# Kernel tuning notes

Measured on AMD Instinct MI355X. Metric: run time of the kernel, lower is better.

Reference implementation:

```python
import jax, jax.numpy as jnp
import numpy as np

V, E, U, B, T = 50000, 128, 256, 256, 1024


def _lstm_cell(x, h, c, W, R, b):
    # Keras LSTMCell gate order: i, f, g(candidate), o
    z = x @ W + h @ R + b  # [B, 4U]
    i, f, g, o = jnp.split(z, 4, axis=-1)
    i = jax.nn.sigmoid(i)
    f = jax.nn.sigmoid(f)
    g = jnp.tanh(g)
    o = jax.nn.sigmoid(o)
    c_new = f * c + i * g
    h_new = o * jnp.tanh(c_new)
    return h_new, c_new


def setup_inputs() -> dict:
    key = jax.random.key(0)
    ks = jax.random.split(key, 10)
    s = lambda k, shape, scale: jax.random.normal(k, shape, dtype=jnp.float32) * scale
    return {
        "tokens": jax.random.randint(ks[0], (B, T), 0, V),
        "emb": s(ks[1], (V, E), 0.05),
        "W0": s(ks[2], (E, 4 * U), 1.0 / np.sqrt(E)),
        "R0": s(ks[3], (U, 4 * U), 1.0 / np.sqrt(U)),
        "b0": jnp.zeros((4 * U,), jnp.float32),
        "W1": s(ks[4], (U, 4 * U), 1.0 / np.sqrt(U)),
        "R1": s(ks[5], (U, 4 * U), 1.0 / np.sqrt(U)),
        "b1": jnp.zeros((4 * U,), jnp.float32),
        "Wout": s(ks[6], (U, 1), 1.0 / np.sqrt(U)),
        "bout": jnp.zeros((1,), jnp.float32),
    }


def reference(tokens, emb, W0, R0, b0, W1, R1, b1, Wout, bout):
    x = emb[tokens]                      # [B, T, E]
    xs = jnp.transpose(x, (1, 0, 2))     # [T, B, E] scan over time
    h0 = jnp.zeros((B, U), x.dtype)
    c0 = jnp.zeros((B, U), x.dtype)
    h1 = jnp.zeros((B, U), x.dtype)
    c1 = jnp.zeros((B, U), x.dtype)

    def step(carry, x_t):
        h0, c0, h1, c1 = carry
        h0, c0 = _lstm_cell(x_t, h0, c0, W0, R0, b0)
        h1, c1 = _lstm_cell(h0, h1, c1, W1, R1, b1)
        return (h0, c0, h1, c1), None

    (h0, c0, h1, c1), _ = jax.lax.scan(step, (h0, c0, h1, c1), xs)
    logits = h1 @ Wout + bout            # [B, 1]
    return jax.nn.sigmoid(logits)
```

## Files before the change

kernel.cpp:

```cpp
#include <hip/hip_runtime.h>

typedef unsigned short u16;
typedef unsigned int u32;
typedef unsigned long long u64;
typedef __attribute__((ext_vector_type(8))) short bf16x8;
typedef __attribute__((ext_vector_type(4))) float f32x4;

#define T_STEPS 1024
#define E_SZ 128
#define U_SZ 256

#define NG 16
#define MB 16
#define NSL 8
#define RD 8
#define HS 264
#define EPAD 136
#define BSTRIDE 192

#define POLL_BAIL 60000

#define L0_W0T 0
#define L0_R0T 32768
#define L0_X   98304
#define L0_STG 102656
#define L0_G   110848
#define L0_B   119616
#define L1_W1T 0
#define L1_R1T 65536
#define L1_SG0 131072
#define L1_SG1 139264
#define L1_G   147456
#define L1_B   156224
#define SMEM_TOTAL 156800

__device__ u64 g_exH0[RD * NG * NSL * BSTRIDE];
__device__ u64 g_exH1[2 * NG * NSL * BSTRIDE];
__device__ int g_pr[NG * NSL * 16];
__device__ u32 g_run;
__device__ int g_isF32;

__device__ __forceinline__ float bf2f(u16 u) {
  union { u32 i; float f; } v; v.i = ((u32)u) << 16; return v.f;
}
__device__ __forceinline__ u16 f2bf(float f) {
  union { u32 i; float f; } v; v.f = f;
  u32 r = v.i + 0x7fffu + ((v.i >> 16) & 1u);
  return (u16)(r >> 16);
}
__device__ __forceinline__ float sig_(float x) { return 1.f / (1.f + __expf(-x)); }
__device__ __forceinline__ float tnh_(float x) { return 2.f / (1.f + __expf(-2.f * x)) - 1.f; }

extern "C" __global__ void dtype_probe(const void* W0v) {
  __shared__ int cntBig;
  if (threadIdx.x == 0) cntBig = 0;
  __syncthreads();
  const u16* u = (const u16*)W0v;
  int big = 0;
  for (int i = threadIdx.x; i < 4096; i += 256)
    if ((u[i] & 0x7F80u) >= 0x4100u) big++;
  atomicAdd(&cntBig, big);
  __syncthreads();
  for (int i = threadIdx.x; i < NG * NSL * 16; i += 256) g_pr[i] = 0;
  if (threadIdx.x == 0) {
    g_isF32 = (cntBig > 100) ? 1 : 0;
    g_run = g_run + 1;
  }
}

__device__ __forceinline__ u64 ldAtom(const u64* p) {
  return __hip_atomic_load(p, __ATOMIC_RELAXED, __HIP_MEMORY_SCOPE_AGENT);
}

__device__ __forceinline__ int wavePollMin(const int* fA, int tgt, int lane,
                                           int& dead) {
  if (dead) return tgt;
  const int* p = (lane < 8) ? fA + lane * 16 : nullptr;
  int ok = (p == nullptr);
  int v = 0x7fffffff;
  int it = 0;
  while (!__all(ok)) {
    if (!ok) {
      v = __hip_atomic_load(p, __ATOMIC_RELAXED, __HIP_MEMORY_SCOPE_AGENT);
      ok = v >= tgt;
    }
    if (++it > POLL_BAIL) { dead = 1; break; }
    if (it > 48) __builtin_amdgcn_s_sleep(1);
  }
  __atomic_signal_fence(__ATOMIC_ACQUIRE);
  int m = (lane < 8) ? v : 0x7fffffff;
#pragma unroll
  for (int off = 4; off; off >>= 1) {
    int o = __shfl_down(m, off);
    m = m < o ? m : o;
  }
  return __shfl(m, 0);
}

__device__ __forceinline__ void unpackToLds(const u64 q0, const u64 q1, const u64 q2,
                                            u16* __restrict__ stg, int slice,
                                            int ml, int quad) {
  u32 a0 = (u32)q0, a1 = (u32)(q0 >> 32);
  u32 b0 = (u32)q1, b1 = (u32)(q1 >> 32);
  u32 c0 = (u32)q2;
  uint4 F;
  F.x = a0;
  F.y = (a1 & 0xFFFFu) | (b0 << 16);
  F.z = (b0 >> 16) | (b1 << 16);
  F.w = c0;
  *(uint4*)(stg + (((slice << 6) + (quad << 4) + ml) << 3)) = F;
}

__device__ __forceinline__ void stageOne(const u64* __restrict__ base, u32 etag,
                                         u16* __restrict__ stg,
                                         int wv, int ml, int quad, int& dead) {
  const int j0 = wv << 1;
  const u64* p0 = base + (u64)j0 * BSTRIDE + ml * 12 + quad * 3;
  const u64* p1 = p0 + BSTRIDE;
  u64 qa0 = ldAtom(p0), qa1 = ldAtom(p0 + 1), qa2 = ldAtom(p0 + 2);
  u64 qb0 = ldAtom(p1), qb1 = ldAtom(p1 + 1), qb2 = ldAtom(p1 + 2);
  int it = 0;
  while (true) {
    u32 badA = (((u32)(qa0 >> 48)) ^ etag) | (((u32)(qa1 >> 48)) ^ etag) |
               (((u32)(qa2 >> 48)) ^ etag);
    u32 badB = (((u32)(qb0 >> 48)) ^ etag) | (((u32)(qb1 >> 48)) ^ etag) |
               (((u32)(qb2 >> 48)) ^ etag);
    if (!__any((badA | badB) != 0)) break;
    if (dead) break;
    if (++it > POLL_BAIL) { dead = 1; break; }
    if (badA) { qa0 = ldAtom(p0); qa1 = ldAtom(p0 + 1); qa2 = ldAtom(p0 + 2); }
    if (badB) { qb0 = ldAtom(p1); qb1 = ldAtom(p1 + 1); qb2 = ldAtom(p1 + 2); }
    if (it > 8) __builtin_amdgcn_s_sleep(1);
  }
  __atomic_signal_fence(__ATOMIC_ACQUIRE);
  unpackToLds(qa0, qa1, qa2, stg, j0, ml, quad);
  unpackToLds(qb0, qb1, qb2, stg, j0 + 1, ml, quad);
}

__device__ __forceinline__ void stageDual(const u64* __restrict__ b0, u32 e0,
                                          u16* __restrict__ s0,
                                          const u64* __restrict__ b1, u32 e1,
                                          u16* __restrict__ s1, int doH1,
                                          int wv, int ml, int quad, int& dead) {
  const int j0 = wv << 1;
  const int off = ml * 12 + quad * 3;
  const u64* p0a = b0 + (u64)j0 * BSTRIDE + off;
  const u64* p0b = p0a + BSTRIDE;
  const u64* p1a = b1 + (u64)j0 * BSTRIDE + off;
  const u64* p1b = p1a + BSTRIDE;
  u64 xa0 = ldAtom(p0a), xa1 = ldAtom(p0a + 1), xa2 = ldAtom(p0a + 2);
  u64 xb0 = ldAtom(p0b), xb1 = ldAtom(p0b + 1), xb2 = ldAtom(p0b + 2);
  u64 ya0 = 0, ya1 = 0, ya2 = 0, yb0 = 0, yb1 = 0, yb2 = 0;
  if (doH1) {
    ya0 = ldAtom(p1a); ya1 = ldAtom(p1a + 1); ya2 = ldAtom(p1a + 2);
    yb0 = ldAtom(p1b); yb1 = ldAtom(p1b + 1); yb2 = ldAtom(p1b + 2);
  }
  int it = 0;
  while (true) {
    u32 badA = (((u32)(xa0 >> 48)) ^ e0) | (((u32)(xa1 >> 48)) ^ e0) |
               (((u32)(xa2 >> 48)) ^ e0);
    u32 badB = (((u32)(xb0 >> 48)) ^ e0) | (((u32)(xb1 >> 48)) ^ e0) |
               (((u32)(xb2 >> 48)) ^ e0);
    u32 badC = 0, badD = 0;
    if (doH1) {
      badC = (((u32)(ya0 >> 48)) ^ e1) | (((u32)(ya1 >> 48)) ^ e1) |
             (((u32)(ya2 >> 48)) ^ e1);
      badD = (((u32)(yb0 >> 48)) ^ e1) | (((u32)(yb1 >> 48)) ^ e1) |
             (((u32)(yb2 >> 48)) ^ e1);
    }
    if (!__any((badA | badB | badC | badD) != 0)) break;
    if (dead) break;
    if (++it > POLL_BAIL) { dead = 1; break; }
    if (badA) { xa0 = ldAtom(p0a); xa1 = ldAtom(p0a + 1); xa2 = ldAtom(p0a + 2); }
    if (badB) { xb0 = ldAtom(p0b); xb1 = ldAtom(p0b + 1); xb2 = ldAtom(p0b + 2); }
    if (badC) { ya0 = ldAtom(p1a); ya1 = ldAtom(p1a + 1); ya2 = ldAtom(p1a + 2); }
    if (badD) { yb0 = ldAtom(p1b); yb1 = ldAtom(p1b + 1); yb2 = ldAtom(p1b + 2); }
    if (it > 8) __builtin_amdgcn_s_sleep(1);
  }
  __atomic_signal_fence(__ATOMIC_ACQUIRE);
  unpackToLds(xa0, xa1, xa2, s0, j0, ml, quad);
  unpackToLds(xb0, xb1, xb2, s0, j0 + 1, ml, quad);
  if (doH1) {
    unpackToLds(ya0, ya1, ya2, s1, j0, ml, quad);
    unpackToLds(yb0, yb1, yb2, s1, j0 + 1, ml, quad);
  }
}

extern "C" __global__ void __launch_bounds__(256, 1)
lstm_fused(const int* __restrict__ tokens, const void* __restrict__ emb,
           const void* __restrict__ W0, const void* __restrict__ R0, const void* __restrict__ b0,
           const void* __restrict__ W1, const void* __restrict__ R1, const void* __restrict__ b1,
           const void* __restrict__ Wout, const void* __restrict__ bout,
           void* __restrict__ outv) {
  extern __shared__ char smem[];

  const int tid = threadIdx.x;
  const int b = blockIdx.x;
  const int g = b & (NG - 1);
  const int w = b >> 4;
  const int role = w >> 3;
  const int sl = w & 7;
  const int isF32 = g_isF32;
  const u32 tagB = ((u32)g_run) << 10;

  auto ldf = [&](const void* p, int idx) -> float {
    return isF32 ? ((const float*)p)[idx] : bf2f(((const u16*)p)[idx]);
  };

  const int lane = tid & 63;
  const int wv = tid >> 6;
  const int ml = lane & 15;
  const int quad = lane >> 4;
  const int um = tid >> 4;
  const int un = tid & 15;
  const int lfr = (quad << 4) + ml;

  const int mB = tid >> 4;
  const int uS = tid & 15;
  const int qS = uS / 3;
  const int sS = uS - qS * 3;
  const int kb = (qS << 3) + 3 * sS;
  const int nFull = (sS != 2);

  int* flp = g_pr + (g << 3) * 16;
  int dead = 0;

  if (role == 0) {
    u16* w0t = (u16*)(smem + L0_W0T);
    u16* r0t = (u16*)(smem + L0_R0T);
    u16* ldsX = (u16*)(smem + L0_X);
    u16* stg = (u16*)(smem + L0_STG);
    float* ldsG = (float*)(smem + L0_G);
    float* ldsB = (float*)(smem + L0_B);

    for (int i = tid; i < 128 * 128; i += 256) {
      int k = i >> 7, n = i & 127;
      int col = ((n >> 5) << 8) + (sl << 5) + (n & 31);
      int wv_ = n >> 5, s_ = (n >> 4) & 1, ml_ = n & 15;
      int j_ = k >> 5, q_ = (k >> 3) & 3, e_ = k & 7;
      int dst = ((((wv_ << 1) + s_) * 4 + j_) * 64 + (q_ << 4) + ml_) * 8 + e_;
      w0t[dst] = f2bf(ldf(W0, k * 1024 + col));
    }
    for (int i = tid; i < 128 * 256; i += 256) {
      int k = i >> 7, n = i & 127;
      int col = ((n >> 5) << 8) + (sl << 5) + (n & 31);
      int wv_ = n >> 5, s_ = (n >> 4) & 1, ml_ = n & 15;
      int j_ = k >> 5, q_ = (k >> 3) & 3, e_ = k & 7;
      int dst = ((((wv_ << 1) + s_) * 8 + j_) * 64 + (q_ << 4) + ml_) * 8 + e_;
      r0t[dst] = f2bf(ldf(R0, k * 1024 + col));
    }
    if (tid < 128) {
      int col = ((tid >> 5) << 8) + (sl << 5) + (tid & 31);
      ldsB[tid] = ldf(b0, col);
    }

    float cst[3] = {0.f, 0.f, 0.f};
    const int tokBase = (g * MB + um) * T_STEPS;
    int prMin = 0;

    float4 xfA, xfB; uint4 xbf;
    {
      int tok = tokens[tokBase];
      if (isF32) {
        const float* row = (const float*)emb + (u64)tok * E_SZ + (un << 3);
        xfA = *(const float4*)row; xfB = *(const float4*)(row + 4);
      } else {
        xbf = *(const uint4*)((const u16*)emb + (u64)tok * E_SZ + (un << 3));
      }
    }
    __syncthreads();

    const int row0 = (wv << 5) + ml;
    const u16* brA0 = w0t + (u32)(((wv << 1) + 0) * 256 + lfr) * 8;
    const u16* brB0 = w0t + (u32)(((wv << 1) + 1) * 256 + lfr) * 8;
    const u16* brA2 = r0t + (u32)(((wv << 1) + 0) * 512 + lfr) * 8;
    const u16* brB2 = r0t + (u32)(((wv << 1) + 1) * 512 + lfr) * 8;

    for (int t = 0; t < T_STEPS; t++) {
      if (t >= RD && prMin < t - RD + 1)
        prMin = wavePollMin(flp, t - RD + 1, lane, dead);

      {
        uint4 pk;
        if (isF32) {
          pk.x = (u32)f2bf(xfA.x) | ((u32)f2bf(xfA.y) << 16);
          pk.y = (u32)f2bf(xfA.z) | ((u32)f2bf(xfA.w) << 16);
          pk.z = (u32)f2bf(xfB.x) | ((u32)f2bf(xfB.y) << 16);
          pk.w = (u32)f2bf(xfB.z) | ((u32)f2bf(xfB.w) << 16);
        } else pk = xbf;
        *(uint4*)(ldsX + um * EPAD + (un << 3)) = pk;
      }
      __syncthreads();

      float ba = ldsB[row0], bb = ldsB[row0 + 16];
      f32x4 acA = {ba, ba, ba, ba}, acB = {bb, bb, bb, bb};

      {
        const u16* ar = ldsX + ml * EPAD + (quad << 3);
#pragma unroll
        for (int kc = 0; kc < 4; kc++) {
          bf16x8 av = *(const bf16x8*)(ar + kc * 32);
          acA = __builtin_amdgcn_mfma_f32_16x16x32_bf16(av, *(const bf16x8*)(brA0 + (kc << 9)), acA, 0, 0, 0);
          acB = __builtin_amdgcn_mfma_f32_16x16x32_bf16(av, *(const bf16x8*)(brB0 + (kc << 9)), acB, 0, 0, 0);
        }
      }

      if (t > 0) {
        const u64* base = g_exH0 +
            (u64)((((t - 1) & (RD - 1)) * NG + g) * NSL) * BSTRIDE;
        stageOne(base, (tagB + t) & 0xFFFFu, stg, wv, ml, quad, dead);
      }
      __syncthreads();

      if (t > 0) {
#pragma unroll
        for (int j = 0; j < NSL; j++) {
          bf16x8 fv = *(const bf16x8*)(stg + (((j << 6) + lfr) << 3));
          acA = __builtin_amdgcn_mfma_f32_16x16x32_bf16(fv, *(const bf16x8*)(brA2 + (j << 9)), acA, 0, 0, 0);
          acB = __builtin_amdgcn_mfma_f32_16x16x32_bf16(fv, *(const bf16x8*)(brB2 + (j << 9)), acB, 0, 0, 0);
        }
      }

#pragma unroll
      for (int r = 0; r < 4; r++) {
        int m = (quad << 2) + r;
        float gA = (wv == 2) ? tnh_(acA[r]) : sig_(acA[r]);
        float gB = (wv == 2) ? tnh_(acB[r]) : sig_(acB[r]);
        ldsG[row0 * 17 + m] = gA;
        ldsG[(row0 + 16) * 17 + m] = gB;
      }
      __syncthreads();

      if (uS < 12) {
        u64 val = ((u64)((tagB + t + 1) & 0xFFFFu)) << 48;
#pragma unroll
        for (int i2 = 0; i2 < 3; i2++) {
          if (i2 < 2 || nFull) {
            int k = kb + i2;
            float iv = ldsG[k * 17 + mB];
            float fv = ldsG[(32 + k) * 17 + mB];
            float gv = ldsG[(64 + k) * 17 + mB];
            float ov = ldsG[(96 + k) * 17 + mB];
            float c = fv * cst[i2] + iv * gv; cst[i2] = c;
            val |= ((u64)f2bf(ov * tnh_(c))) << (16 * i2);
          }
        }
        u64 elem = (u64)(((t & (RD - 1)) * NG + g) * NSL + sl) * BSTRIDE +
                   mB * 12 + uS;
        __hip_atomic_store(g_exH0 + elem, val,
                           __ATOMIC_RELAXED, __HIP_MEMORY_SCOPE_AGENT);
      }

      if (t + 1 < T_STEPS) {
        int tok = tokens[tokBase + t + 1];
        if (isF32) {
          const float* row = (const float*)emb + (u64)tok * E_SZ + (un << 3);
          xfA = *(const float4*)row; xfB = *(const float4*)(row + 4);
        } else {
          xbf = *(const uint4*)((const u16*)emb + (u64)tok * E_SZ + (un << 3));
        }
      }
    }
  } else {
    u16* w1t = (u16*)(smem + L1_W1T);
    u16* r1t = (u16*)(smem + L1_R1T);
    u16* stg0 = (u16*)(smem + L1_SG0);
    u16* stg1 = (u16*)(smem + L1_SG1);
    float* ldsG = (float*)(smem + L1_G);
    float* ldsB = (float*)(smem + L1_B);

    for (int i = tid; i < 128 * 256; i += 256) {
      int k = i >> 7, n = i & 127;
      int col = ((n >> 5) << 8) + (sl << 5) + (n & 31);
      int wv_ = n >> 5, s_ = (n >> 4) & 1, ml_ = n & 15;
      int j_ = k >> 5, q_ = (k >> 3) & 3, e_ = k & 7;
      int dst = ((((wv_ << 1) + s_) * 8 + j_) * 64 + (q_ << 4) + ml_) * 8 + e_;
      w1t[dst] = f2bf(ldf(W1, k * 1024 + col));
      r1t[dst] = f2bf(ldf(R1, k * 1024 + col));
    }
    if (tid < 128) {
      int col = ((tid >> 5) << 8) + (sl << 5) + (tid & 31);
      ldsB[tid] = ldf(b1, col);
    }
    __syncthreads();

    float cst[3] = {0.f, 0.f, 0.f};
    const int row0 = (wv << 5) + ml;
    const u16* brA1 = w1t + (u32)(((wv << 1) + 0) * 512 + lfr) * 8;
    const u16* brB1 = w1t + (u32)(((wv << 1) + 1) * 512 + lfr) * 8;
    const u16* brA2 = r1t + (u32)(((wv << 1) + 0) * 512 + lfr) * 8;
    const u16* brB2 = r1t + (u32)(((wv << 1) + 1) * 512 + lfr) * 8;

    for (int t = 0; t < T_STEPS; t++) {
      {
        const u64* h0base = g_exH0 +
            (u64)(((t & (RD - 1)) * NG + g) * NSL) * BSTRIDE;
        const u64* h1base = g_exH1 +
            (u64)((((t - 1) & 1) * NG + g) * NSL) * BSTRIDE;
        stageDual(h0base, (tagB + t + 1) & 0xFFFFu, stg0,
                  h1base, (tagB + t) & 0xFFFFu, stg1, (t > 0),
                  wv, ml, quad, dead);
      }
      __syncthreads();

      if (tid == 0) {
        __atomic_signal_fence(__ATOMIC_RELEASE);
        __hip_atomic_store(g_pr + ((g << 3) + sl) * 16, t + 1,
                           __ATOMIC_RELAXED, __HIP_MEMORY_SCOPE_AGENT);
      }

      float ba = ldsB[row0], bb = ldsB[row0 + 16];
      f32x4 acA = {ba, ba, ba, ba}, acB = {bb, bb, bb, bb};

#pragma unroll
      for (int j = 0; j < NSL; j++) {
        bf16x8 fv = *(const bf16x8*)(stg0 + (((j << 6) + lfr) << 3));
        acA = __builtin_amdgcn_mfma_f32_16x16x32_bf16(fv, *(const bf16x8*)(brA1 + (j << 9)), acA, 0, 0, 0);
        acB = __builtin_amdgcn_mfma_f32_16x16x32_bf16(fv, *(const bf16x8*)(brB1 + (j << 9)), acB, 0, 0, 0);
      }
      if (t > 0) {
#pragma unroll
        for (int j = 0; j < NSL; j++) {
          bf16x8 fv = *(const bf16x8*)(stg1 + (((j << 6) + lfr) << 3));
          acA = __builtin_amdgcn_mfma_f32_16x16x32_bf16(fv, *(const bf16x8*)(brA2 + (j << 9)), acA, 0, 0, 0);
          acB = __builtin_amdgcn_mfma_f32_16x16x32_bf16(fv, *(const bf16x8*)(brB2 + (j << 9)), acB, 0, 0, 0);
        }
      }

#pragma unroll
      for (int r = 0; r < 4; r++) {
        int m = (quad << 2) + r;
        float gA = (wv == 2) ? tnh_(acA[r]) : sig_(acA[r]);
        float gB = (wv == 2) ? tnh_(acB[r]) : sig_(acB[r]);
        ldsG[row0 * 17 + m] = gA;
        ldsG[(row0 + 16) * 17 + m] = gB;
      }
      __syncthreads();

      if (uS < 12) {
        u64 val = ((u64)((tagB + t + 1) & 0xFFFFu)) << 48;
#pragma unroll
        for (int i2 = 0; i2 < 3; i2++) {
          if (i2 < 2 || nFull) {
            int k = kb + i2;
            float iv = ldsG[k * 17 + mB];
            float fv = ldsG[(32 + k) * 17 + mB];
            float gv = ldsG[(64 + k) * 17 + mB];
            float ov = ldsG[(96 + k) * 17 + mB];
            float c = fv * cst[i2] + iv * gv; cst[i2] = c;
            val |= ((u64)f2bf(ov * tnh_(c))) << (16 * i2);
          }
        }
        u64 elem = (u64)(((t & 1) * NG + g) * NSL + sl) * BSTRIDE +
                   mB * 12 + uS;
        __hip_atomic_store(g_exH1 + elem, val,
                           __ATOMIC_RELAXED, __HIP_MEMORY_SCOPE_AGENT);
      }
      __syncthreads();
    }

    if (sl == 0) {
      u16* ldsEpi = stg0;
      const u32 etag = (tagB + T_STEPS) & 0xFFFFu;
      if (uS < 12) {
        for (int sp = 0; sp < 8; sp++) {
          const u64* p = g_exH1 +
              (u64)(((1) * NG + g) * NSL + sp) * BSTRIDE + mB * 12 + uS;
          u64 v; int it = 0;
          while (true) {
            v = ldAtom(p);
            if ((u32)(v >> 48) == etag) break;
            if (dead) break;
            if (++it > POLL_BAIL) { dead = 1; break; }
            if (it > 8) __builtin_amdgcn_s_sleep(1);
          }
          u16* dst = ldsEpi + mB * HS + (sp << 5) + kb;
          dst[0] = (u16)v;
          dst[1] = (u16)(v >> 16);
          if (nFull) dst[2] = (u16)(v >> 32);
        }
      }
      __syncthreads();
      float* woutf = ldsG;
      float* red = ldsG + 272;
      woutf[tid] = ldf(Wout, tid);
      __syncthreads();
      float p = 0.f;
#pragma unroll
      for (int j = 0; j < 16; j++)
        p += bf2f(ldsEpi[um * HS + (un << 4) + j]) * woutf[(un << 4) + j];
      red[um * 17 + un] = p;
      __syncthreads();
      if (tid < 16) {
        float sum = ldf(bout, 0);
#pragma unroll
        for (int j = 0; j < 16; j++) sum += red[tid * 17 + j];
        float val = sig_(sum);
        if (isF32) ((float*)outv)[g * MB + tid] = val;
        else       ((u16*)outv)[g * MB + tid] = f2bf(val);
      }
    }
  }
}

extern "C" void kernel_launch(void* const* d_in, const int* in_sizes, int n_in,
                              void* d_out, int out_size, void* d_ws, size_t ws_size,
                              hipStream_t stream) {
  const int* tokens = (const int*)d_in[0];
  const void* emb  = d_in[1];
  const void* W0   = d_in[2];
  const void* R0   = d_in[3];
  const void* b0   = d_in[4];
  const void* W1   = d_in[5];
  const void* R1   = d_in[6];
  const void* b1   = d_in[7];
  const void* Wout = d_in[8];
  const void* bout = d_in[9];

  hipFuncSetAttribute((const void*)lstm_fused,
                      hipFuncAttributeMaxDynamicSharedMemorySize, SMEM_TOTAL);

  dtype_probe<<<dim3(1), dim3(256), 0, stream>>>(W0);

  lstm_fused<<<dim3(256), dim3(256), SMEM_TOTAL, stream>>>(
      tokens, emb, W0, R0, b0, W1, R1, b1, Wout, bout, d_out);
}
```

Baseline: 3.182 ms.

## Overlap layer-1 recurrent MFMA with h0 polling and keep own slice local

Layer 1 now stages and computes the h1·R1 half of the gates before waiting for the fresh h0 from layer 0, so the recurrent matmul overlaps the cross-block dependency. Each block also writes its own freshly computed h slice directly into its LDS staging buffer and skips polling global memory for that slice, in both layers. Layer-0 global loads for the previous h0 are issued earlier, before the input MFMA, so their latency overlaps compute. One per-step __syncthreads at the end of the layer-1 loop is removed. This adds more intricate ordering between LDS writes and the next step's reads, which raises the risk of races.

```diff
diff --git a/kernel.cpp b/kernel.cpp
--- a/kernel.cpp
+++ b/kernel.cpp
@@ -97,6 +97,11 @@
   return __shfl(m, 0);
 }
 
+__device__ __forceinline__ u32 tagBad(u64 a, u64 b, u64 c, u32 etag) {
+  return (((u32)(a >> 48)) ^ etag) | (((u32)(b >> 48)) ^ etag) |
+         (((u32)(c >> 48)) ^ etag);
+}
+
 __device__ __forceinline__ void unpackToLds(const u64 q0, const u64 q1, const u64 q2,
                                             u16* __restrict__ stg, int slice,
                                             int ml, int quad) {
@@ -111,79 +116,23 @@
   *(uint4*)(stg + (((slice << 6) + (quad << 4) + ml) << 3)) = F;
 }
 
-__device__ __forceinline__ void stageOne(const u64* __restrict__ base, u32 etag,
-                                         u16* __restrict__ stg,
-                                         int wv, int ml, int quad, int& dead) {
-  const int j0 = wv << 1;
-  const u64* p0 = base + (u64)j0 * BSTRIDE + ml * 12 + quad * 3;
-  const u64* p1 = p0 + BSTRIDE;
-  u64 qa0 = ldAtom(p0), qa1 = ldAtom(p0 + 1), qa2 = ldAtom(p0 + 2);
-  u64 qb0 = ldAtom(p1), qb1 = ldAtom(p1 + 1), qb2 = ldAtom(p1 + 2);
+__device__ __forceinline__ void pollPair(const u64* __restrict__ pA,
+                                         const u64* __restrict__ pB,
+                                         u32 etag, int skip,
+                                         u64& a0, u64& a1, u64& a2,
+                                         u64& b0, u64& b1, u64& b2, int& dead) {
   int it = 0;
   while (true) {
-    u32 badA = (((u32)(qa0 >> 48)) ^ etag) | (((u32)(qa1 >> 48)) ^ etag) |
-               (((u32)(qa2 >> 48)) ^ etag);
-    u32 badB = (((u32)(qb0 >> 48)) ^ etag) | (((u32)(qb1 >> 48)) ^ etag) |
-               (((u32)(qb2 >> 48)) ^ etag);
+    u32 badA = (skip == 0) ? 0u : tagBad(a0, a1, a2, etag);
+    u32 badB = (skip == 1) ? 0u : tagBad(b0, b1, b2, etag);
     if (!__any((badA | badB) != 0)) break;
     if (dead) break;
     if (++it > POLL_BAIL) { dead = 1; break; }
-    if (badA) { qa0 = ldAtom(p0); qa1 = ldAtom(p0 + 1); qa2 = ldAtom(p0 + 2); }
-    if (badB) { qb0 = ldAtom(p1); qb1 = ldAtom(p1 + 1); qb2 = ldAtom(p1 + 2); }
+    if (badA) { a0 = ldAtom(pA); a1 = ldAtom(pA + 1); a2 = ldAtom(pA + 2); }
+    if (badB) { b0 = ldAtom(pB); b1 = ldAtom(pB + 1); b2 = ldAtom(pB + 2); }
     if (it > 8) __builtin_amdgcn_s_sleep(1);
   }
   __atomic_signal_fence(__ATOMIC_ACQUIRE);
-  unpackToLds(qa0, qa1, qa2, stg, j0, ml, quad);
-  unpackToLds(qb0, qb1, qb2, stg, j0 + 1, ml, quad);
-}
-
-__device__ __forceinline__ void stageDual(const u64* __restrict__ b0, u32 e0,
-                                          u16* __restrict__ s0,
-                                          const u64* __restrict__ b1, u32 e1,
-                                          u16* __restrict__ s1, int doH1,
-                                          int wv, int ml, int quad, int& dead) {
-  const int j0 = wv << 1;
-  const int off = ml * 12 + quad * 3;
-  const u64* p0a = b0 + (u64)j0 * BSTRIDE + off;
-  const u64* p0b = p0a + BSTRIDE;
-  const u64* p1a = b1 + (u64)j0 * BSTRIDE + off;
-  const u64* p1b = p1a + BSTRIDE;
-  u64 xa0 = ldAtom(p0a), xa1 = ldAtom(p0a + 1), xa2 = ldAtom(p0a + 2);
-  u64 xb0 = ldAtom(p0b), xb1 = ldAtom(p0b + 1), xb2 = ldAtom(p0b + 2);
-  u64 ya0 = 0, ya1 = 0, ya2 = 0, yb0 = 0, yb1 = 0, yb2 = 0;
-  if (doH1) {
-    ya0 = ldAtom(p1a); ya1 = ldAtom(p1a + 1); ya2 = ldAtom(p1a + 2);
-    yb0 = ldAtom(p1b); yb1 = ldAtom(p1b + 1); yb2 = ldAtom(p1b + 2);
-  }
-  int it = 0;
-  while (true) {
-    u32 badA = (((u32)(xa0 >> 48)) ^ e0) | (((u32)(xa1 >> 48)) ^ e0) |
-               (((u32)(xa2 >> 48)) ^ e0);
-    u32 badB = (((u32)(xb0 >> 48)) ^ e0) | (((u32)(xb1 >> 48)) ^ e0) |
-               (((u32)(xb2 >> 48)) ^ e0);
-    u32 badC = 0, badD = 0;
-    if (doH1) {
-      badC = (((u32)(ya0 >> 48)) ^ e1) | (((u32)(ya1 >> 48)) ^ e1) |
-             (((u32)(ya2 >> 48)) ^ e1);
-      badD = (((u32)(yb0 >> 48)) ^ e1) | (((u32)(yb1 >> 48)) ^ e1) |
-             (((u32)(yb2 >> 48)) ^ e1);
-    }
-    if (!__any((badA | badB | badC | badD) != 0)) break;
-    if (dead) break;
-    if (++it > POLL_BAIL) { dead = 1; break; }
-    if (badA) { xa0 = ldAtom(p0a); xa1 = ldAtom(p0a + 1); xa2 = ldAtom(p0a + 2); }
-    if (badB) { xb0 = ldAtom(p0b); xb1 = ldAtom(p0b + 1); xb2 = ldAtom(p0b + 2); }
-    if (badC) { ya0 = ldAtom(p1a); ya1 = ldAtom(p1a + 1); ya2 = ldAtom(p1a + 2); }
-    if (badD) { yb0 = ldAtom(p1b); yb1 = ldAtom(p1b + 1); yb2 = ldAtom(p1b + 2); }
-    if (it > 8) __builtin_amdgcn_s_sleep(1);
-  }
-  __atomic_signal_fence(__ATOMIC_ACQUIRE);
-  unpackToLds(xa0, xa1, xa2, s0, j0, ml, quad);
-  unpackToLds(xb0, xb1, xb2, s0, j0 + 1, ml, quad);
-  if (doH1) {
-    unpackToLds(ya0, ya1, ya2, s1, j0, ml, quad);
-    unpackToLds(yb0, yb1, yb2, s1, j0 + 1, ml, quad);
-  }
 }
 
 extern "C" __global__ void __launch_bounds__(256, 1)
@@ -214,6 +163,7 @@
   const int um = tid >> 4;
   const int un = tid & 15;
   const int lfr = (quad << 4) + ml;
+  const int slotOwn = ((sl >> 1) == wv) ? (sl & 1) : -1;
 
   const int mB = tid >> 4;
   const int uS = tid & 15;
@@ -292,6 +242,17 @@
       }
       __syncthreads();
 
+      u64 qa0 = 0, qa1 = 0, qa2 = 0, qb0 = 0, qb1 = 0, qb2 = 0;
+      const u64* gp0 = nullptr; const u64* gp1 = nullptr;
+      if (t > 0) {
+        const u64* base = g_exH0 +
+            (u64)((((t - 1) & (RD - 1)) * NG + g) * NSL) * BSTRIDE;
+        gp0 = base + (u64)(wv << 1) * BSTRIDE + ml * 12 + quad * 3;
+        gp1 = gp0 + BSTRIDE;
+        if (slotOwn != 0) { qa0 = ldAtom(gp0); qa1 = ldAtom(gp0 + 1); qa2 = ldAtom(gp0 + 2); }
+        if (slotOwn != 1) { qb0 = ldAtom(gp1); qb1 = ldAtom(gp1 + 1); qb2 = ldAtom(gp1 + 2); }
+      }
+
       float ba = ldsB[row0], bb = ldsB[row0 + 16];
       f32x4 acA = {ba, ba, ba, ba}, acB = {bb, bb, bb, bb};
 
@@ -306,9 +267,10 @@
       }
 
       if (t > 0) {
-        const u64* base = g_exH0 +
-            (u64)((((t - 1) & (RD - 1)) * NG + g) * NSL) * BSTRIDE;
-        stageOne(base, (tagB + t) & 0xFFFFu, stg, wv, ml, quad, dead);
+        pollPair(gp0, gp1, (tagB + t) & 0xFFFFu, slotOwn,
+                 qa0, qa1, qa2, qb0, qb1, qb2, dead);
+        if (slotOwn != 0) unpackToLds(qa0, qa1, qa2, stg, (wv << 1), ml, quad);
+        if (slotOwn != 1) unpackToLds(qb0, qb1, qb2, stg, (wv << 1) + 1, ml, quad);
       }
       __syncthreads();
 
@@ -333,6 +295,7 @@
 
       if (uS < 12) {
         u64 val = ((u64)((tagB + t + 1) & 0xFFFFu)) << 48;
+        u16 hw0 = 0, hw1 = 0, hw2 = 0;
 #pragma unroll
         for (int i2 = 0; i2 < 3; i2++) {
           if (i2 < 2 || nFull) {
@@ -342,9 +305,14 @@
             float gv = ldsG[(64 + k) * 17 + mB];
             float ov = ldsG[(96 + k) * 17 + mB];
             float c = fv * cst[i2] + iv * gv; cst[i2] = c;
-            val |= ((u64)f2bf(ov * tnh_(c))) << (16 * i2);
+            u16 hh = f2bf(ov * tnh_(c));
+            if (i2 == 0) hw0 = hh; else if (i2 == 1) hw1 = hh; else hw2 = hh;
+            val |= ((u64)hh) << (16 * i2);
           }
         }
+        u16* own = stg + (((sl << 6) + (qS << 4) + mB) << 3) + 3 * sS;
+        own[0] = hw0; own[1] = hw1;
+        if (nFull) own[2] = hw2;
         u64 elem = (u64)(((t & (RD - 1)) * NG + g) * NSL + sl) * BSTRIDE +
                    mB * 12 + uS;
         __hip_atomic_store(g_exH0 + elem, val,
@@ -392,15 +360,51 @@
     const u16* brB2 = r1t + (u32)(((wv << 1) + 1) * 512 + lfr) * 8;
 
     for (int t = 0; t < T_STEPS; t++) {
-      {
-        const u64* h0base = g_exH0 +
-            (u64)(((t & (RD - 1)) * NG + g) * NSL) * BSTRIDE;
-        const u64* h1base = g_exH1 +
-            (u64)((((t - 1) & 1) * NG + g) * NSL) * BSTRIDE;
-        stageDual(h0base, (tagB + t + 1) & 0xFFFFu, stg0,
-                  h1base, (tagB + t) & 0xFFFFu, stg1, (t > 0),
-                  wv, ml, quad, dead);
-      }
+      const u32 e1 = (tagB + t) & 0xFFFFu;
+      const u32 e0 = (tagB + t + 1) & 0xFFFFu;
+      const int off = ml * 12 + quad * 3;
+      const u64* h1b = g_exH1 +
+          (u64)((((t - 1) & 1) * NG + g) * NSL) * BSTRIDE;
+      const u64* h0b = g_exH0 +
+          (u64)(((t & (RD - 1)) * NG + g) * NSL) * BSTRIDE;
+      const u64* p1a = h1b + (u64)(wv << 1) * BSTRIDE + off;
+      const u64* p1b = p1a + BSTRIDE;
+      const u64* p0a = h0b + (u64)(wv << 1) * BSTRIDE + off;
+      const u64* p0b = p0a + BSTRIDE;
+
+      u64 ya0 = 0, ya1 = 0, ya2 = 0, yb0 = 0, yb1 = 0, yb2 = 0;
+      if (t > 0) {
+        if (slotOwn != 0) { ya0 = ldAtom(p1a); ya1 = ldAtom(p1a + 1); ya2 = ldAtom(p1a + 2); }
+        if (slotOwn != 1) { yb0 = ldAtom(p1b); yb1 = ldAtom(p1b + 1); yb2 = ldAtom(p1b + 2); }
+      }
+      u64 xa0 = ldAtom(p0a), xa1 = ldAtom(p0a + 1), xa2 = ldAtom(p0a + 2);
+      u64 xb0 = ldAtom(p0b), xb1 = ldAtom(p0b + 1), xb2 = ldAtom(p0b + 2);
+
+      if (t > 0) {
+        pollPair(p1a, p1b, e1, slotOwn, ya0, ya1, ya2, yb0, yb1, yb2, dead);
+        if (slotOwn != 0) unpackToLds(ya0, ya1, ya2, stg1, (wv << 1), ml, quad);
+        if (slotOwn != 1) unpackToLds(yb0, yb1, yb2, stg1, (wv << 1) + 1, ml, quad);
+      }
+      __syncthreads();
+
+      if (tagBad(xa0, xa1, xa2, e0)) { xa0 = ldAtom(p0a); xa1 = ldAtom(p0a + 1); xa2 = ldAtom(p0a + 2); }
+      if (tagBad(xb0, xb1, xb2, e0)) { xb0 = ldAtom(p0b); xb1 = ldAtom(p0b + 1); xb2 = ldAtom(p0b + 2); }
+
+      float ba = ldsB[row0], bb = ldsB[row0 + 16];
+      f32x4 acA = {ba, ba, ba, ba}, acB = {bb, bb, bb, bb};
+
+      if (t > 0) {
+#pragma unroll
+        for (int j = 0; j < NSL; j++) {
+          bf16x8 fv = *(const bf16x8*)(stg1 + (((j << 6) + lfr) << 3));
+          acA = __builtin_amdgcn_mfma_f32_16x16x32_bf16(fv, *(const bf16x8*)(brA2 + (j << 9)), acA, 0, 0, 0);
+          acB = __builtin_amdgcn_mfma_f32_16x16x32_bf16(fv, *(const bf16x8*)(brB2 + (j << 9)), acB, 0, 0, 0);
+        }
+      }
+
+      pollPair(p0a, p0b, e0, -1, xa0, xa1, xa2, xb0, xb1, xb2, dead);
+      unpackToLds(xa0, xa1, xa2, stg0, (wv << 1), ml, quad);
+      unpackToLds(xb0, xb1, xb2, stg0, (wv << 1) + 1, ml, quad);
       __syncthreads();
 
       if (tid == 0) {
@@ -409,22 +413,11 @@
                            __ATOMIC_RELAXED, __HIP_MEMORY_SCOPE_AGENT);
       }
 
-      float ba = ldsB[row0], bb = ldsB[row0 + 16];
-      f32x4 acA = {ba, ba, ba, ba}, acB = {bb, bb, bb, bb};
-
 #pragma unroll
       for (int j = 0; j < NSL; j++) {
         bf16x8 fv = *(const bf16x8*)(stg0 + (((j << 6) + lfr) << 3));
         acA = __builtin_amdgcn_mfma_f32_16x16x32_bf16(fv, *(const bf16x8*)(brA1 + (j << 9)), acA, 0, 0, 0);
         acB = __builtin_amdgcn_mfma_f32_16x16x32_bf16(fv, *(const bf16x8*)(brB1 + (j << 9)), acB, 0, 0, 0);
-      }
-      if (t > 0) {
-#pragma unroll
-        for (int j = 0; j < NSL; j++) {
-          bf16x8 fv = *(const bf16x8*)(stg1 + (((j << 6) + lfr) << 3));
-          acA = __builtin_amdgcn_mfma_f32_16x16x32_bf16(fv, *(const bf16x8*)(brA2 + (j << 9)), acA, 0, 0, 0);
-          acB = __builtin_amdgcn_mfma_f32_16x16x32_bf16(fv, *(const bf16x8*)(brB2 + (j << 9)), acB, 0, 0, 0);
-        }
       }
 
 #pragma unroll
@@ -439,6 +432,7 @@
 
       if (uS < 12) {
         u64 val = ((u64)((tagB + t + 1) & 0xFFFFu)) << 48;
+        u16 hw0 = 0, hw1 = 0, hw2 = 0;
 #pragma unroll
         for (int i2 = 0; i2 < 3; i2++) {
           if (i2 < 2 || nFull) {
@@ -448,18 +442,23 @@
             float gv = ldsG[(64 + k) * 17 + mB];
             float ov = ldsG[(96 + k) * 17 + mB];
             float c = fv * cst[i2] + iv * gv; cst[i2] = c;
-            val |= ((u64)f2bf(ov * tnh_(c))) << (16 * i2);
+            u16 hh = f2bf(ov * tnh_(c));
+            if (i2 == 0) hw0 = hh; else if (i2 == 1) hw1 = hh; else hw2 = hh;
+            val |= ((u64)hh) << (16 * i2);
           }
         }
+        u16* own = stg1 + (((sl << 6) + (qS << 4) + mB) << 3) + 3 * sS;
+        own[0] = hw0; own[1] = hw1;
+        if (nFull) own[2] = hw2;
         u64 elem = (u64)(((t & 1) * NG + g) * NSL + sl) * BSTRIDE +
                    mB * 12 + uS;
         __hip_atomic_store(g_exH1 + elem, val,
                            __ATOMIC_RELAXED, __HIP_MEMORY_SCOPE_AGENT);
       }
-      __syncthreads();
     }
 
     if (sl == 0) {
+      __syncthreads();
       u16* ldsEpi = stg0;
       const u32 etag = (tagB + T_STEPS) & 0xFFFFu;
       if (uS < 12) {
```

Measured after the change: 4.248 ms. 33.5% more time.
